# Kernel optimization log

Measured on AMD Instinct MI355X. Metric: run time of the kernel, lower is better.

Reference implementation:

```python
import jax, jax.numpy as jnp
import numpy as np

# Dims: L layers, batch B, seq S, model dim D, heads H, ffn FF
L, B, S, D, H = 8, 2, 1024, 1024, 16
FF = 4 * D
HD = D // H
EPS = 1e-5  # torch LayerNorm default


def setup_inputs() -> dict:
    key = jax.random.key(0)
    ks = jax.random.split(key, 6)
    g = lambda k, shape, s: jax.random.normal(k, shape, jnp.float32) * s
    return {
        "x": g(ks[0], (B, S, D), 1.0),
        # True = masked out (code passes ~attn_mask to F.sdpa): causal mask
        "attn_mask": jnp.triu(jnp.ones((S, S), bool), 1),
        "qkv_w": g(ks[1], (L, 3 * D, D), 0.02),
        "qkv_b": jnp.zeros((L, 3 * D), jnp.float32),
        "out_w": g(ks[2], (L, D, D), 0.02),
        "out_b": jnp.zeros((L, D), jnp.float32),
        "w1": g(ks[3], (L, FF, D), 0.02),
        "b1": jnp.zeros((L, FF), jnp.float32),
        "w2": g(ks[4], (L, D, FF), 0.02),
        "b2": jnp.zeros((L, D), jnp.float32),
        "ln1_w": jnp.ones((L, D), jnp.float32),
        "ln1_b": jnp.zeros((L, D), jnp.float32),
        "ln2_w": jnp.ones((L, D), jnp.float32),
        "ln2_b": jnp.zeros((L, D), jnp.float32),
    }


def _layer_norm(x, w, b):
    m = jnp.mean(x, axis=-1, keepdims=True)
    v = jnp.var(x, axis=-1, keepdims=True)
    return (x - m) * jax.lax.rsqrt(v + EPS) * w + b


def _block(x, mask, qw, qb, ow, ob, w1, b1, w2, b2, l1w, l1b, l2w, l2b):
    # fused QKV projection: [B,S,3D]
    qkv = jnp.einsum("bsd,ed->bse", x, qw) + qb
    q, k, v = jnp.split(qkv, 3, axis=-1)
    k_cache, v_cache = k, v  # caches are stored pre-head-split [B,S,D]
    to_heads = lambda t: t.reshape(B, S, H, HD).transpose(0, 2, 1, 3)
    qh, kh, vh = to_heads(q), to_heads(k), to_heads(v)
    scores = jnp.einsum("bhqd,bhkd->bhqk", qh, kh) / jnp.sqrt(jnp.float32(HD))
    scores = jnp.where(mask, -jnp.inf, scores)  # mask True = disallowed
    attn = jnp.einsum("bhqk,bhkd->bhqd", jax.nn.softmax(scores, axis=-1), vh)
    attn = attn.transpose(0, 2, 1, 3).reshape(B, S, D)
    attn = jnp.einsum("bsd,ed->bse", attn, ow) + ob
    # post-LN residual + ReLU MLP + post-LN (padding_mask=None branch)
    x = _layer_norm(x + attn, l1w, l1b)
    h = jnp.einsum("bsf,df->bsd", jax.nn.relu(jnp.einsum("bsd,fd->bsf", x, w1) + b1), w2) + b2
    x = _layer_norm(x + h, l2w, l2b)
    return x, k_cache, v_cache


def reference(x, attn_mask, qkv_w, qkv_b, out_w, out_b, w1, b1, w2, b2,
              ln1_w, ln1_b, ln2_w, ln2_b):
    def step(carry, p):
        xc = carry
        xo, kc, vc = _block(xc, attn_mask, *p)
        return xo, (kc, vc)

    params = (qkv_w, qkv_b, out_w, out_b, w1, b1, w2, b2,
              ln1_w, ln1_b, ln2_w, ln2_b)
    x_out, (k_cache, v_cache) = jax.lax.scan(step, x, params)
    return x_out, k_cache, v_cache
```

## Files before the change

### kernel.cpp

```cpp
#include <hip/hip_runtime.h>
#include <cstdint>
#include <cstddef>
#include <math.h>

#define LL  8
#define BB  2
#define SS  1024
#define DD  1024
#define HH  16
#define HD  64
#define FFD 4096
#define BSD (BB*SS*DD)

typedef __attribute__((ext_vector_type(4))) float f32x4;
typedef __attribute__((ext_vector_type(8))) short bf16x8;
typedef __attribute__((ext_vector_type(4))) short bf16x4;

__device__ __forceinline__ unsigned short f2bf(float f) {
    unsigned u = __float_as_uint(f);
    unsigned r = (u + 0x7fffu + ((u >> 16) & 1u)) >> 16;
    return (unsigned short)r;
}
__device__ __forceinline__ float bf2f(unsigned short u) {
    return __uint_as_float((unsigned)u << 16);
}

#define GLD16(gsrc, ldst) \
    __builtin_amdgcn_global_load_lds((const __attribute__((address_space(1))) void*)(gsrc), \
                                     (__attribute__((address_space(3))) void*)(ldst), 16, 0, 0)

__device__ __forceinline__ void xcd_swizzle(int& bx, int& by)
{
    const int nx  = gridDim.x;
    const int nwg = nx * gridDim.y;
    const int flat = by * nx + bx;
    const int cpx = nwg >> 3;
    const int swz = (flat & 7) * cpx + (flat >> 3);
    bx = swz % nx;
    by = swz / nx;
}

__global__ __launch_bounds__(256)
void cvt_bf16(const float* __restrict__ in, unsigned short* __restrict__ out)
{
    size_t i = (size_t)blockIdx.x * 256 + threadIdx.x;
    float4 v = *(const float4*)(in + i * 4);
    ushort4 o;
    o.x = f2bf(v.x); o.y = f2bf(v.y); o.z = f2bf(v.z); o.w = f2bf(v.w);
    *(ushort4*)(out + i * 4) = o;
}

__global__ __launch_bounds__(256)
void cvt_x(const float* __restrict__ in, float* __restrict__ outf,
           unsigned short* __restrict__ outb)
{
    size_t i = (size_t)blockIdx.x * 256 + threadIdx.x;
    float4 v = *(const float4*)(in + i * 4);
    *(float4*)(outf + i * 4) = v;
    ushort4 o;
    o.x = f2bf(v.x); o.y = f2bf(v.y); o.z = f2bf(v.z); o.w = f2bf(v.w);
    *(ushort4*)(outb + i * 4) = o;
}

__global__ __launch_bounds__(512)
void gemm_bf16(const unsigned short* __restrict__ A, const unsigned short* __restrict__ W,
               const float* __restrict__ bias,
               float* __restrict__ C, unsigned short* __restrict__ Cb,
               float* __restrict__ Ck, float* __restrict__ Cv,
               unsigned short* __restrict__ Kb16, unsigned short* __restrict__ Vb16,
               int M, int N, int klen, int mode)
{
    __shared__ unsigned short lds[2][2 * 128 * 64];

    int bx = blockIdx.x, by = blockIdx.y;
    xcd_swizzle(bx, by);

    const int tid  = threadIdx.x;
    const int m0   = by * 128;
    const int n0   = bx * 128;
    const int kbase= blockIdx.z * klen;
    const int lane = tid & 63;
    const int w    = tid >> 6;
    const int wr   = w >> 2;
    const int wc   = w & 3;
    const int lr   = lane & 15;
    const int kq   = lane >> 4;

    const int K = (mode == 3) ? (klen * gridDim.z) : klen;
    const int T = klen >> 6;

    const int srow0 = tid >> 3;
    const int spc0  = tid & 7;
    const int slc0  = spc0 ^ (srow0 & 7);
    const int srow1 = (tid + 512) >> 3;
    const int spc1  = (tid + 512) & 7;
    const int slc1  = spc1 ^ (srow1 & 7);

    #define STAGE_TILE(ti, dst)                                                   \
        do {                                                                      \
            const int kc = kbase + (ti) * 64;                                     \
            GLD16(A + (size_t)(m0 + srow0) * K + kc + slc0 * 8, (dst) + tid * 8); \
            GLD16(A + (size_t)(m0 + srow1) * K + kc + slc1 * 8, (dst) + 4096 + tid * 8); \
            GLD16(W + (size_t)(n0 + srow0) * K + kc + slc0 * 8, (dst) + 8192 + tid * 8); \
            GLD16(W + (size_t)(n0 + srow1) * K + kc + slc1 * 8, (dst) + 12288 + tid * 8); \
        } while (0)

    f32x4 acc[4][2];
    #pragma unroll
    for (int i = 0; i < 4; ++i)
        #pragma unroll
        for (int j = 0; j < 2; ++j) {
            f32x4 z = {0.f, 0.f, 0.f, 0.f};
            acc[i][j] = z;
        }

    STAGE_TILE(0, lds[0]);
    STAGE_TILE(1, lds[1]);

    for (int t = 0; t < T; ++t) {
        unsigned short* cb = lds[t & 1];

        if (t == T - 1) {
            asm volatile("s_waitcnt vmcnt(0)\n\ts_barrier" ::: "memory");
        } else {
            asm volatile("s_waitcnt vmcnt(4)\n\ts_barrier" ::: "memory");
        }

        bf16x8 a[4], b[2], a2[4], b2[2];
        #pragma unroll
        for (int mf = 0; mf < 4; ++mf) {
            const int r = wr * 64 + mf * 16 + lr;
            const int pc = kq ^ (r & 7);
            a[mf] = *(const bf16x8*)(cb + r * 64 + pc * 8);
        }
        #pragma unroll
        for (int nf = 0; nf < 2; ++nf) {
            const int r = wc * 32 + nf * 16 + lr;
            const int pc = kq ^ (r & 7);
            b[nf] = *(const bf16x8*)(cb + 8192 + r * 64 + pc * 8);
        }
        #pragma unroll
        for (int mf = 0; mf < 4; ++mf) {
            const int r = wr * 64 + mf * 16 + lr;
            const int pc = (4 + kq) ^ (r & 7);
            a2[mf] = *(const bf16x8*)(cb + r * 64 + pc * 8);
        }
        #pragma unroll
        for (int nf = 0; nf < 2; ++nf) {
            const int r = wc * 32 + nf * 16 + lr;
            const int pc = (4 + kq) ^ (r & 7);
            b2[nf] = *(const bf16x8*)(cb + 8192 + r * 64 + pc * 8);
        }

        __builtin_amdgcn_s_setprio(1);
        #pragma unroll
        for (int mf = 0; mf < 4; ++mf)
            #pragma unroll
            for (int nf = 0; nf < 2; ++nf)
                acc[mf][nf] = __builtin_amdgcn_mfma_f32_16x16x32_bf16(
                    a[mf], b[nf], acc[mf][nf], 0, 0, 0);
        #pragma unroll
        for (int mf = 0; mf < 4; ++mf)
            #pragma unroll
            for (int nf = 0; nf < 2; ++nf)
                acc[mf][nf] = __builtin_amdgcn_mfma_f32_16x16x32_bf16(
                    a2[mf], b2[nf], acc[mf][nf], 0, 0, 0);
        __builtin_amdgcn_s_setprio(0);

        asm volatile("s_waitcnt lgkmcnt(0)\n\ts_barrier" ::: "memory");
        if (t + 2 < T) STAGE_TILE(t + 2, cb);
    }
    #undef STAGE_TILE

    const int seg = n0 >> 10;
    #pragma unroll
    for (int nf = 0; nf < 2; ++nf) {
        const int cl = wc * 32 + nf * 16 + lr;
        const float bv = (mode == 3) ? 0.f : bias[n0 + cl];
        #pragma unroll
        for (int mf = 0; mf < 4; ++mf) {
            #pragma unroll
            for (int r = 0; r < 4; ++r) {
                const int row = m0 + wr * 64 + mf * 16 + kq * 4 + r;
                const float val = acc[mf][nf][r] + bv;
                if (mode == 2) {
                    const int col = (n0 & 1023) + cl;
                    float* dstf = (seg == 1) ? Ck : ((seg == 2) ? Cv : nullptr);
                    unsigned short* dstb = (seg == 0) ? Cb : ((seg == 1) ? Kb16 : Vb16);
                    if (dstf) dstf[(size_t)row * DD + col] = val;
                    dstb[(size_t)row * DD + col] = f2bf(val);
                } else if (mode == 1) {
                    Cb[(size_t)row * N + n0 + cl] = f2bf(fmaxf(val, 0.f));
                } else {
                    Cb[(size_t)blockIdx.z * M * N + (size_t)row * N + n0 + cl] = f2bf(val);
                }
            }
        }
    }
}

__global__ __launch_bounds__(512)
void attn_mfma(const unsigned short* __restrict__ Qb, const unsigned short* __restrict__ Kb,
               const unsigned short* __restrict__ Vb, unsigned short* __restrict__ ctxb)
{
    int bx = blockIdx.x, by = blockIdx.y;
    xcd_swizzle(bx, by);
    const int qt = bx;
    const int h  = by;
    const int b  = blockIdx.z;
    const int tid  = threadIdx.x;
    const int lane = tid & 63;
    const int w    = tid >> 6;
    const int lr   = lane & 15;
    const int hi   = lane >> 4;

    __shared__ unsigned short smem[128 * 68 + 64 * 136 + 8 * 16 * 136];
    unsigned short* Ks = smem;
    unsigned short* Vt = smem + 128 * 68;
    unsigned short* Pl = smem + 128 * 68 + 64 * 136 + w * 16 * 136;

    const int qg0 = qt * 128 + w * 16;

    bf16x8 qa[2];
    {
        const unsigned short* qp = Qb + ((size_t)(b * SS + qg0 + lr)) * DD + h * HD;
        qa[0] = *(const bf16x8*)(qp + hi * 8);
        qa[1] = *(const bf16x8*)(qp + 32 + hi * 8);
    }

    f32x4 accO[4];
    #pragma unroll
    for (int t = 0; t < 4; ++t) { f32x4 z = {0.f,0.f,0.f,0.f}; accO[t] = z; }
    float m_run[4], l_run[4];
    #pragma unroll
    for (int r = 0; r < 4; ++r) { m_run[r] = -INFINITY; l_run[r] = 0.f; }

    const int nch = qt + 1;
    for (int c = 0; c < nch; ++c) {
        __syncthreads();
        const unsigned short* kb = Kb + ((size_t)(b * SS + c * 128)) * DD + h * HD;
        const unsigned short* vb = Vb + ((size_t)(b * SS + c * 128)) * DD + h * HD;
        #pragma unroll
        for (int i = 0; i < 2; ++i) {
            int e = tid + i * 512;
            int r  = e >> 3, ch = e & 7;
            bf16x8 kv = *(const bf16x8*)(kb + (size_t)r * DD + ch * 8);
            *(bf16x4*)(Ks + r * 68 + ch * 8)     = __builtin_shufflevector(kv, kv, 0,1,2,3);
            *(bf16x4*)(Ks + r * 68 + ch * 8 + 4) = __builtin_shufflevector(kv, kv, 4,5,6,7);
            int k  = e & 127, d0 = (e >> 7) * 8;
            bf16x8 vv = *(const bf16x8*)(vb + (size_t)k * DD + d0);
            #pragma unroll
            for (int j = 0; j < 8; ++j)
                Vt[(d0 + j) * 136 + k] = (unsigned short)vv[j];
        }
        __syncthreads();

        f32x4 sa[8];
        #pragma unroll
        for (int t = 0; t < 8; ++t) { f32x4 z = {0.f,0.f,0.f,0.f}; sa[t] = z; }
        #pragma unroll
        for (int t = 0; t < 8; ++t) {
            #pragma unroll
            for (int s = 0; s < 2; ++s) {
                const unsigned short* bp = Ks + (t * 16 + lr) * 68 + s * 32 + hi * 8;
                bf16x4 b0 = *(const bf16x4*)bp;
                bf16x4 b1 = *(const bf16x4*)(bp + 4);
                bf16x8 bb = __builtin_shufflevector(b0, b1, 0,1,2,3,4,5,6,7);
                sa[t] = __builtin_amdgcn_mfma_f32_16x16x32_bf16(qa[s], bb, sa[t], 0, 0, 0);
            }
        }
        #pragma unroll
        for (int t = 0; t < 8; ++t) {
            #pragma unroll
            for (int r = 0; r < 4; ++r) {
                const int kg = c * 128 + t * 16 + lr;
                const int qg = qg0 + hi * 4 + r;
                sa[t][r] = (kg > qg) ? -1e30f : sa[t][r] * 0.125f;
            }
        }
        #pragma unroll
        for (int r = 0; r < 4; ++r) {
            float mx = -INFINITY;
            #pragma unroll
            for (int t = 0; t < 8; ++t) mx = fmaxf(mx, sa[t][r]);
            mx = fmaxf(mx, __shfl_xor(mx, 1));
            mx = fmaxf(mx, __shfl_xor(mx, 2));
            mx = fmaxf(mx, __shfl_xor(mx, 4));
            mx = fmaxf(mx, __shfl_xor(mx, 8));
            const float mn = fmaxf(m_run[r], mx);
            float sum = 0.f;
            #pragma unroll
            for (int t = 0; t < 8; ++t) {
                float p = __expf(sa[t][r] - mn);
                sa[t][r] = p;
                sum += p;
            }
            sum += __shfl_xor(sum, 1);
            sum += __shfl_xor(sum, 2);
            sum += __shfl_xor(sum, 4);
            sum += __shfl_xor(sum, 8);
            const float sc = __expf(m_run[r] - mn);
            l_run[r] = l_run[r] * sc + sum;
            m_run[r] = mn;
            #pragma unroll
            for (int t = 0; t < 4; ++t) accO[t][r] *= sc;
        }
        #pragma unroll
        for (int t = 0; t < 8; ++t)
            #pragma unroll
            for (int r = 0; r < 4; ++r)
                Pl[(hi * 4 + r) * 136 + t * 16 + lr] = f2bf(sa[t][r]);

        #pragma unroll
        for (int s = 0; s < 4; ++s) {
            const unsigned short* ap = Pl + lr * 136 + s * 32 + hi * 8;
            bf16x4 a0 = *(const bf16x4*)ap;
            bf16x4 a1 = *(const bf16x4*)(ap + 4);
            bf16x8 aa = __builtin_shufflevector(a0, a1, 0,1,2,3,4,5,6,7);
            #pragma unroll
            for (int t = 0; t < 4; ++t) {
                const unsigned short* bp = Vt + (t * 16 + lr) * 136 + s * 32 + hi * 8;
                bf16x4 b0 = *(const bf16x4*)bp;
                bf16x4 b1 = *(const bf16x4*)(bp + 4);
                bf16x8 bb = __builtin_shufflevector(b0, b1, 0,1,2,3,4,5,6,7);
                accO[t] = __builtin_amdgcn_mfma_f32_16x16x32_bf16(aa, bb, accO[t], 0, 0, 0);
            }
        }
    }

    float inv[4];
    #pragma unroll
    for (int r = 0; r < 4; ++r) inv[r] = 1.f / l_run[r];

    __syncthreads();
    float* Of = (float*)smem;
    #pragma unroll
    for (int t = 0; t < 4; ++t)
        #pragma unroll
        for (int r = 0; r < 4; ++r)
            Of[(w * 16 + hi * 4 + r) * 68 + t * 16 + lr] = accO[t][r] * inv[r];
    __syncthreads();
    #pragma unroll
    for (int i = 0; i < 2; ++i) {
        int e = tid + i * 512;
        int r = e >> 3, ch = e & 7;
        const float* src = Of + r * 68 + ch * 8;
        float4 v0 = *(const float4*)(src);
        float4 v1 = *(const float4*)(src + 4);
        bf16x8 o;
        o[0] = (short)f2bf(v0.x); o[1] = (short)f2bf(v0.y);
        o[2] = (short)f2bf(v0.z); o[3] = (short)f2bf(v0.w);
        o[4] = (short)f2bf(v1.x); o[5] = (short)f2bf(v1.y);
        o[6] = (short)f2bf(v1.z); o[7] = (short)f2bf(v1.w);
        *(bf16x8*)(ctxb + ((size_t)(b * SS + qt * 128 + r)) * DD + h * HD + ch * 8) = o;
    }
}

__global__ __launch_bounds__(256)
void ln_kernel(const float* __restrict__ x, float* __restrict__ xo,
               const unsigned short* __restrict__ P,
               const float* __restrict__ bias,
               const float* __restrict__ w, const float* __restrict__ b,
               unsigned short* __restrict__ xb)
{
    const size_t PS = (size_t)BSD;
    const int row = blockIdx.x;
    const int t   = threadIdx.x;
    const int d0  = t * 4;
    const float* xr = x + (size_t)row * DD;
    float* xor_ = xo + (size_t)row * DD;
    unsigned short* xbr = xb + (size_t)row * DD;
    const size_t base = (size_t)row * DD + d0;

    float4 xv = *(const float4*)(xr + d0);
    float4 bv = *(const float4*)(bias + d0);
    float z[4] = {xv.x + bv.x, xv.y + bv.y, xv.z + bv.z, xv.w + bv.w};
    #pragma unroll
    for (int p = 0; p < 4; ++p) {
        ushort4 pv = *(const ushort4*)(P + base + p * PS);
        z[0] += bf2f(pv.x); z[1] += bf2f(pv.y); z[2] += bf2f(pv.z); z[3] += bf2f(pv.w);
    }
    float s = z[0] + z[1] + z[2] + z[3];
    float ss = z[0]*z[0] + z[1]*z[1] + z[2]*z[2] + z[3]*z[3];

    #pragma unroll
    for (int off = 32; off; off >>= 1) {
        s  += __shfl_down(s, off);
        ss += __shfl_down(ss, off);
    }
    __shared__ float sbuf[4], ssbuf[4];
    const int wave = t >> 6, lane = t & 63;
    if (lane == 0) { sbuf[wave] = s; ssbuf[wave] = ss; }
    __syncthreads();
    if (t == 0) {
        float S = 0.f, SSum = 0.f;
        #pragma unroll
        for (int i = 0; i < 4; ++i) { S += sbuf[i]; SSum += ssbuf[i]; }
        float mean = S * (1.f / 1024.f);
        float var  = SSum * (1.f / 1024.f) - mean * mean;
        sbuf[0]  = mean;
        ssbuf[0] = rsqrtf(var + 1e-5f);
    }
    __syncthreads();
    const float mean = sbuf[0], rstd = ssbuf[0];

    float4 wv = *(const float4*)(w + d0);
    float4 bb = *(const float4*)(b + d0);
    float o0 = (z[0] - mean) * rstd * wv.x + bb.x;
    float o1 = (z[1] - mean) * rstd * wv.y + bb.y;
    float o2 = (z[2] - mean) * rstd * wv.z + bb.z;
    float o3 = (z[3] - mean) * rstd * wv.w + bb.w;
    *(float4*)(xor_ + d0) = make_float4(o0, o1, o2, o3);
    ushort4 ob4;
    ob4.x = f2bf(o0); ob4.y = f2bf(o1); ob4.z = f2bf(o2); ob4.w = f2bf(o3);
    *(ushort4*)(xbr + d0) = ob4;
}

extern "C" void kernel_launch(void* const* d_in, const int* in_sizes, int n_in,
                              void* d_out, int out_size, void* d_ws, size_t ws_size,
                              hipStream_t stream)
{
    const float* x_in  = (const float*)d_in[0];
    const float* qkv_w = (const float*)d_in[2];
    const float* qkv_b = (const float*)d_in[3];
    const float* out_w = (const float*)d_in[4];
    const float* out_b = (const float*)d_in[5];
    const float* w1    = (const float*)d_in[6];
    const float* b1    = (const float*)d_in[7];
    const float* w2    = (const float*)d_in[8];
    const float* b2    = (const float*)d_in[9];
    const float* ln1w  = (const float*)d_in[10];
    const float* ln1b  = (const float*)d_in[11];
    const float* ln2w  = (const float*)d_in[12];
    const float* ln2b  = (const float*)d_in[13];

    float* out_x = (float*)d_out;
    float* out_k = out_x + (size_t)BSD;
    float* out_v = out_k + (size_t)LL * BSD;

    const size_t MEG = 1024 * 1024;
    float* ws = (float*)d_ws;
    float*          xbuf  = ws;
    unsigned short* part16= (unsigned short*)(ws + 2 * MEG);
    unsigned short* xb16  = (unsigned short*)(ws + 6 * MEG);
    unsigned short* ctxb  = (unsigned short*)(ws + 7 * MEG);
    unsigned short* hb16  = (unsigned short*)(ws + 8 * MEG);
    unsigned short* qb16  = hb16;
    unsigned short* kb16  = hb16 + 2 * MEG;
    unsigned short* vb16  = hb16 + 4 * MEG;
    unsigned short* wAll  = (unsigned short*)(ws + 12 * MEG);

    unsigned short* qkvW = wAll;
    unsigned short* outW = wAll + 24 * MEG;
    unsigned short* w1W  = wAll + 32 * MEG;
    unsigned short* w2W  = wAll + 64 * MEG;

    cvt_bf16<<<24 * MEG / 1024, 256, 0, stream>>>(qkv_w, qkvW);
    cvt_bf16<<< 8 * MEG / 1024, 256, 0, stream>>>(out_w, outW);
    cvt_bf16<<<32 * MEG / 1024, 256, 0, stream>>>(w1,    w1W);
    cvt_bf16<<<32 * MEG / 1024, 256, 0, stream>>>(w2,    w2W);
    cvt_x<<<BSD / 1024, 256, 0, stream>>>(x_in, xbuf, xb16);

    const int M = BB * SS;

    for (int l = 0; l < LL; ++l) {
        const float* qb  = qkv_b + (size_t)l * 3 * DD;
        const float* ob  = out_b + (size_t)l * DD;
        const float* b1l = b1    + (size_t)l * FFD;
        const float* b2l = b2    + (size_t)l * DD;
        const unsigned short* qwl = qkvW + (size_t)l * 3 * DD * DD;
        const unsigned short* owl = outW + (size_t)l * DD * DD;
        const unsigned short* w1l = w1W  + (size_t)l * FFD * DD;
        const unsigned short* w2l = w2W  + (size_t)l * DD * FFD;
        float* kc = out_k + (size_t)l * BSD;
        float* vc = out_v + (size_t)l * BSD;

        gemm_bf16<<<dim3(3 * DD / 128, M / 128, 1), 512, 0, stream>>>(
            xb16, qwl, qb, nullptr, qb16, kc, vc, kb16, vb16, M, 3 * DD, DD, 2);

        attn_mfma<<<dim3(SS / 128, HH, BB), 512, 0, stream>>>(qb16, kb16, vb16, ctxb);

        gemm_bf16<<<dim3(DD / 128, M / 128, 4), 512, 0, stream>>>(
            ctxb, owl, nullptr, nullptr, part16, nullptr, nullptr, nullptr, nullptr,
            M, DD, DD / 4, 3);

        ln_kernel<<<M, 256, 0, stream>>>(xbuf, xbuf, part16, ob,
                                         ln1w + (size_t)l * DD, ln1b + (size_t)l * DD, xb16);

        gemm_bf16<<<dim3(FFD / 128, M / 128, 1), 512, 0, stream>>>(
            xb16, w1l, b1l, nullptr, hb16, nullptr, nullptr, nullptr, nullptr,
            M, FFD, DD, 1);

        gemm_bf16<<<dim3(DD / 128, M / 128, 4), 512, 0, stream>>>(
            hb16, w2l, nullptr, nullptr, part16, nullptr, nullptr, nullptr, nullptr,
            M, DD, FFD / 4, 3);

        float* xo = (l == LL - 1) ? out_x : xbuf;
        ln_kernel<<<M, 256, 0, stream>>>(xbuf, xo, part16, b2l,
                                         ln2w + (size_t)l * DD, ln2b + (size_t)l * DD, xb16);
    }
}
```

Before: 1.245 ms.

## Enlarge GEMM tile to 256x128 with 8 M-fragments per warp

Doubles the M dimension of the bf16 GEMM block tile from 128 to 256. Each warp now computes 128x32 outputs, and the LDS staging and load pattern are restructured to match. This raises operand reuse per LDS byte and cuts global traffic for the weight tiles. The cost is fewer blocks per launch, which can leave CUs idle, plus higher register and LDS use per block.

```diff
diff --git a/kernel.cpp b/kernel.cpp
--- a/kernel.cpp
+++ b/kernel.cpp
@@ -70,44 +70,43 @@
                unsigned short* __restrict__ Kb16, unsigned short* __restrict__ Vb16,
                int M, int N, int klen, int mode)
 {
-    __shared__ unsigned short lds[2][2 * 128 * 64];
+    __shared__ unsigned short lds[2][(256 + 128) * 64];
 
     int bx = blockIdx.x, by = blockIdx.y;
     xcd_swizzle(bx, by);
 
     const int tid  = threadIdx.x;
-    const int m0   = by * 128;
+    const int m0   = by * 256;
     const int n0   = bx * 128;
     const int kbase= blockIdx.z * klen;
     const int lane = tid & 63;
     const int w    = tid >> 6;
-    const int wr   = w >> 2;
-    const int wc   = w & 3;
+    const int wrM  = w >> 2;
+    const int wcN  = w & 3;
     const int lr   = lane & 15;
     const int kq   = lane >> 4;
 
     const int K = (mode == 3) ? (klen * gridDim.z) : klen;
     const int T = klen >> 6;
 
-    const int srow0 = tid >> 3;
-    const int spc0  = tid & 7;
-    const int slc0  = spc0 ^ (srow0 & 7);
-    const int srow1 = (tid + 512) >> 3;
-    const int spc1  = (tid + 512) & 7;
-    const int slc1  = spc1 ^ (srow1 & 7);
-
-    #define STAGE_TILE(ti, dst)                                                   \
-        do {                                                                      \
-            const int kc = kbase + (ti) * 64;                                     \
-            GLD16(A + (size_t)(m0 + srow0) * K + kc + slc0 * 8, (dst) + tid * 8); \
-            GLD16(A + (size_t)(m0 + srow1) * K + kc + slc1 * 8, (dst) + 4096 + tid * 8); \
-            GLD16(W + (size_t)(n0 + srow0) * K + kc + slc0 * 8, (dst) + 8192 + tid * 8); \
-            GLD16(W + (size_t)(n0 + srow1) * K + kc + slc1 * 8, (dst) + 12288 + tid * 8); \
+    const int sr  = tid >> 3;
+    const int spc = tid & 7;
+    const int slc = spc ^ (sr & 7);
+
+    #define STAGE_TILE(ti, dst)                                                        \
+        do {                                                                           \
+            const int kc = kbase + (ti) * 64;                                          \
+            GLD16(A + (size_t)(m0 + sr      ) * K + kc + slc * 8, (dst) + tid * 8);    \
+            GLD16(A + (size_t)(m0 + sr +  64) * K + kc + slc * 8, (dst) + (tid + 512) * 8); \
+            GLD16(A + (size_t)(m0 + sr + 128) * K + kc + slc * 8, (dst) + (tid + 1024) * 8); \
+            GLD16(A + (size_t)(m0 + sr + 192) * K + kc + slc * 8, (dst) + (tid + 1536) * 8); \
+            GLD16(W + (size_t)(n0 + sr      ) * K + kc + slc * 8, (dst) + 16384 + tid * 8);  \
+            GLD16(W + (size_t)(n0 + sr +  64) * K + kc + slc * 8, (dst) + 16384 + (tid + 512) * 8); \
         } while (0)
 
-    f32x4 acc[4][2];
-    #pragma unroll
-    for (int i = 0; i < 4; ++i)
+    f32x4 acc[8][2];
+    #pragma unroll
+    for (int i = 0; i < 8; ++i)
         #pragma unroll
         for (int j = 0; j < 2; ++j) {
             f32x4 z = {0.f, 0.f, 0.f, 0.f};
@@ -123,49 +122,33 @@
         if (t == T - 1) {
             asm volatile("s_waitcnt vmcnt(0)\n\ts_barrier" ::: "memory");
         } else {
-            asm volatile("s_waitcnt vmcnt(4)\n\ts_barrier" ::: "memory");
-        }
-
-        bf16x8 a[4], b[2], a2[4], b2[2];
-        #pragma unroll
-        for (int mf = 0; mf < 4; ++mf) {
-            const int r = wr * 64 + mf * 16 + lr;
-            const int pc = kq ^ (r & 7);
-            a[mf] = *(const bf16x8*)(cb + r * 64 + pc * 8);
-        }
-        #pragma unroll
-        for (int nf = 0; nf < 2; ++nf) {
-            const int r = wc * 32 + nf * 16 + lr;
-            const int pc = kq ^ (r & 7);
-            b[nf] = *(const bf16x8*)(cb + 8192 + r * 64 + pc * 8);
-        }
-        #pragma unroll
-        for (int mf = 0; mf < 4; ++mf) {
-            const int r = wr * 64 + mf * 16 + lr;
-            const int pc = (4 + kq) ^ (r & 7);
-            a2[mf] = *(const bf16x8*)(cb + r * 64 + pc * 8);
-        }
-        #pragma unroll
-        for (int nf = 0; nf < 2; ++nf) {
-            const int r = wc * 32 + nf * 16 + lr;
-            const int pc = (4 + kq) ^ (r & 7);
-            b2[nf] = *(const bf16x8*)(cb + 8192 + r * 64 + pc * 8);
-        }
-
-        __builtin_amdgcn_s_setprio(1);
-        #pragma unroll
-        for (int mf = 0; mf < 4; ++mf)
-            #pragma unroll
-            for (int nf = 0; nf < 2; ++nf)
-                acc[mf][nf] = __builtin_amdgcn_mfma_f32_16x16x32_bf16(
-                    a[mf], b[nf], acc[mf][nf], 0, 0, 0);
-        #pragma unroll
-        for (int mf = 0; mf < 4; ++mf)
-            #pragma unroll
-            for (int nf = 0; nf < 2; ++nf)
-                acc[mf][nf] = __builtin_amdgcn_mfma_f32_16x16x32_bf16(
-                    a2[mf], b2[nf], acc[mf][nf], 0, 0, 0);
-        __builtin_amdgcn_s_setprio(0);
+            asm volatile("s_waitcnt vmcnt(6)\n\ts_barrier" ::: "memory");
+        }
+
+        #pragma unroll
+        for (int kk = 0; kk < 2; ++kk) {
+            bf16x8 a[8], b[2];
+            #pragma unroll
+            for (int mf = 0; mf < 8; ++mf) {
+                const int r = wrM * 128 + mf * 16 + lr;
+                const int pc = (kk * 4 + kq) ^ (r & 7);
+                a[mf] = *(const bf16x8*)(cb + r * 64 + pc * 8);
+            }
+            #pragma unroll
+            for (int nf = 0; nf < 2; ++nf) {
+                const int r = wcN * 32 + nf * 16 + lr;
+                const int pc = (kk * 4 + kq) ^ (r & 7);
+                b[nf] = *(const bf16x8*)(cb + 16384 + r * 64 + pc * 8);
+            }
+            __builtin_amdgcn_s_setprio(1);
+            #pragma unroll
+            for (int mf = 0; mf < 8; ++mf)
+                #pragma unroll
+                for (int nf = 0; nf < 2; ++nf)
+                    acc[mf][nf] = __builtin_amdgcn_mfma_f32_16x16x32_bf16(
+                        a[mf], b[nf], acc[mf][nf], 0, 0, 0);
+            __builtin_amdgcn_s_setprio(0);
+        }
 
         asm volatile("s_waitcnt lgkmcnt(0)\n\ts_barrier" ::: "memory");
         if (t + 2 < T) STAGE_TILE(t + 2, cb);
@@ -175,13 +158,13 @@
     const int seg = n0 >> 10;
     #pragma unroll
     for (int nf = 0; nf < 2; ++nf) {
-        const int cl = wc * 32 + nf * 16 + lr;
+        const int cl = wcN * 32 + nf * 16 + lr;
         const float bv = (mode == 3) ? 0.f : bias[n0 + cl];
         #pragma unroll
-        for (int mf = 0; mf < 4; ++mf) {
+        for (int mf = 0; mf < 8; ++mf) {
             #pragma unroll
             for (int r = 0; r < 4; ++r) {
-                const int row = m0 + wr * 64 + mf * 16 + kq * 4 + r;
+                const int row = m0 + wrM * 128 + mf * 16 + kq * 4 + r;
                 const float val = acc[mf][nf][r] + bv;
                 if (mode == 2) {
                     const int col = (n0 & 1023) + cl;
@@ -475,23 +458,23 @@
         float* kc = out_k + (size_t)l * BSD;
         float* vc = out_v + (size_t)l * BSD;
 
-        gemm_bf16<<<dim3(3 * DD / 128, M / 128, 1), 512, 0, stream>>>(
+        gemm_bf16<<<dim3(3 * DD / 128, M / 256, 1), 512, 0, stream>>>(
             xb16, qwl, qb, nullptr, qb16, kc, vc, kb16, vb16, M, 3 * DD, DD, 2);
 
         attn_mfma<<<dim3(SS / 128, HH, BB), 512, 0, stream>>>(qb16, kb16, vb16, ctxb);
 
-        gemm_bf16<<<dim3(DD / 128, M / 128, 4), 512, 0, stream>>>(
+        gemm_bf16<<<dim3(DD / 128, M / 256, 4), 512, 0, stream>>>(
             ctxb, owl, nullptr, nullptr, part16, nullptr, nullptr, nullptr, nullptr,
             M, DD, DD / 4, 3);
 
         ln_kernel<<<M, 256, 0, stream>>>(xbuf, xbuf, part16, ob,
                                          ln1w + (size_t)l * DD, ln1b + (size_t)l * DD, xb16);
 
-        gemm_bf16<<<dim3(FFD / 128, M / 128, 1), 512, 0, stream>>>(
+        gemm_bf16<<<dim3(FFD / 128, M / 256, 1), 512, 0, stream>>>(
             xb16, w1l, b1l, nullptr, hb16, nullptr, nullptr, nullptr, nullptr,
             M, FFD, DD, 1);
 
-        gemm_bf16<<<dim3(DD / 128, M / 128, 4), 512, 0, stream>>>(
+        gemm_bf16<<<dim3(DD / 128, M / 256, 4), 512, 0, stream>>>(
             hb16, w2l, nullptr, nullptr, part16, nullptr, nullptr, nullptr, nullptr,
             M, DD, FFD / 4, 3);
 
```

Result: slower. 1.320 ms (+6.0%).
